# Kernel optimization log

Hardware: AMD Instinct MI355X
Metric: run time of the kernel (lower is better)

Reference implementation:

```python
import jax, jax.numpy as jnp
import numpy as np

INPUT_SIZE = 34
HIDDEN = 4
NUM_CLASSES = 3
B, T = 4096, 200


def setup_inputs() -> dict:
    key = jax.random.key(0)
    ks = jax.random.split(key, 8)
    k = 1.0 / np.sqrt(HIDDEN)  # torch default uniform init bound
    u = lambda kk, shape: jax.random.uniform(kk, shape, jnp.float32, -k, k)
    x = jax.random.normal(ks[0], (B, T, INPUT_SIZE), jnp.float32)
    W_ih = u(ks[1], (4 * HIDDEN, INPUT_SIZE))   # gate order: i, f, g, o
    W_hh = u(ks[2], (4 * HIDDEN, HIDDEN))
    b_ih = u(ks[3], (4 * HIDDEN,))
    b_hh = u(ks[4], (4 * HIDDEN,))
    W_fc = u(ks[5], (NUM_CLASSES, HIDDEN))
    b_fc = u(ks[6], (NUM_CLASSES,))
    return {"x": x, "W_ih": W_ih, "W_hh": W_hh, "b_ih": b_ih,
            "b_hh": b_hh, "W_fc": W_fc, "b_fc": b_fc}


def reference(x, W_ih, W_hh, b_ih, b_hh, W_fc, b_fc):
    Bsz = x.shape[0]
    H = W_hh.shape[1]
    # Precompute input contributions for all timesteps: [B, T, 4H]
    x_gates = jnp.einsum('btd,gd->btg', x, W_ih) + b_ih + b_hh
    x_gates = jnp.swapaxes(x_gates, 0, 1)  # [T, B, 4H] for scan

    def step(carry, xg_t):
        h, c = carry
        gates = xg_t + h @ W_hh.T          # [B, 4H]
        i, f, g, o = jnp.split(gates, 4, axis=-1)
        i = jax.nn.sigmoid(i)
        f = jax.nn.sigmoid(f)
        g = jnp.tanh(g)
        o = jax.nn.sigmoid(o)
        c = f * c + i * g
        h = o * jnp.tanh(c)
        return (h, c), None

    h0 = jnp.zeros((Bsz, H), x.dtype)
    c0 = jnp.zeros((Bsz, H), x.dtype)
    (h_last, _), _ = jax.lax.scan(step, (h0, c0), x_gates)
    # dropout is identity in eval mode
    return h_last @ W_fc.T + b_fc  # [B, num_classes]
```

## Files before the change

kernel.cpp:

```cpp
#include <hip/hip_runtime.h>
#include <hip/hip_fp16.h>

#define B_SZ 4096
#define T_SZ 200
#define IN_SZ 34
#define TILES (B_SZ * T_SZ / 64)
#define XG_BLOCKS 1024
#define WAVES_TOTAL (XG_BLOCKS * 2)
#define WT_FLOATS 560

__device__ __forceinline__ float sigf(float x) {
    return 1.0f / (1.0f + __expf(-x));
}
__device__ __forceinline__ float tanh_f(float x) {
    return 2.0f / (1.0f + __expf(-2.0f * x)) - 1.0f;
}

__device__ __forceinline__ float quad_bcast0(float v) {
    int s = __float_as_int(v);
    return __int_as_float(__builtin_amdgcn_update_dpp(s, s, 0x00, 0xf, 0xf, true));
}
__device__ __forceinline__ float quad_bcast1(float v) {
    int s = __float_as_int(v);
    return __int_as_float(__builtin_amdgcn_update_dpp(s, s, 0x55, 0xf, 0xf, true));
}
__device__ __forceinline__ float quad_bcast2(float v) {
    int s = __float_as_int(v);
    return __int_as_float(__builtin_amdgcn_update_dpp(s, s, 0xAA, 0xf, 0xf, true));
}
__device__ __forceinline__ float quad_bcast3(float v) {
    int s = __float_as_int(v);
    return __int_as_float(__builtin_amdgcn_update_dpp(s, s, 0xFF, 0xf, 0xf, true));
}

typedef const __attribute__((address_space(1))) unsigned int* gas_t;
typedef __attribute__((address_space(3))) unsigned int* las_t;

__global__ __launch_bounds__(64) void prep_kernel(
    const float* __restrict__ W_ih, const float* __restrict__ b_ih,
    const float* __restrict__ b_hh, float* __restrict__ wt) {
  for (int i = threadIdx.x; i < WT_FLOATS; i += 64) {
    if (i < 544) {
      int k = i >> 4, g = i & 15;
      wt[i] = W_ih[g * IN_SZ + k];
    } else {
      wt[i] = b_ih[i - 544] + b_hh[i - 544];
    }
  }
}

__global__ __launch_bounds__(128) void xgates_kernel(
    const float* __restrict__ x, const float* __restrict__ wt,
    __half* __restrict__ xg) {
  __shared__ float xs[2 * 2 * 64 * IN_SZ];
  const int lane = threadIdx.x & 63;
  const int wv = threadIdx.x >> 6;
  float* buf0 = &xs[wv * 2 * 64 * IN_SZ];
  float* buf1 = buf0 + 64 * IN_SZ;
  const int gw = blockIdx.x * 2 + wv;

  float bias[16];
  #pragma unroll
  for (int g = 0; g < 16; ++g) bias[g] = wt[544 + g];

  auto issue = [&](int tile, float* buf) {
    const float4* src = reinterpret_cast<const float4*>(x + (size_t)tile * 64 * IN_SZ);
    char* l = reinterpret_cast<char*>(buf);
    #pragma unroll
    for (int i = 0; i < 8; ++i)
      __builtin_amdgcn_global_load_lds((gas_t)(src + i * 64 + lane),
                                       (las_t)(l + i * 1024), 16, 0, 0);
    if (lane < 32)
      __builtin_amdgcn_global_load_lds((gas_t)(src + 512 + lane),
                                       (las_t)(l + 8192), 16, 0, 0);
  };

  int tile = gw;
  if (tile < TILES) issue(tile, buf0);
  int cur = 0;
  #pragma unroll 1
  for (; tile < TILES; tile += WAVES_TOTAL) {
    int nxt = tile + WAVES_TOTAL;
    if (nxt < TILES) {
      issue(nxt, cur ? buf0 : buf1);
      asm volatile("s_waitcnt vmcnt(9)" ::: "memory");
    } else {
      asm volatile("s_waitcnt vmcnt(0)" ::: "memory");
    }
    __builtin_amdgcn_sched_barrier(0);

    const float* buf = cur ? buf1 : buf0;
    float xr[IN_SZ];
    const float2* rp = reinterpret_cast<const float2*>(buf + lane * IN_SZ);
    #pragma unroll
    for (int k = 0; k < IN_SZ / 2; ++k) {
      float2 v = rp[k];
      xr[2 * k] = v.x;
      xr[2 * k + 1] = v.y;
    }
    float acc[16];
    #pragma unroll
    for (int g = 0; g < 16; ++g) acc[g] = bias[g];
    #pragma unroll
    for (int k = 0; k < IN_SZ; ++k) {
      #pragma unroll
      for (int g = 0; g < 16; ++g)
        acc[g] = fmaf(xr[k], wt[k * 16 + g], acc[g]);
    }
    unsigned r = (unsigned)tile * 64u + (unsigned)lane;
    unsigned bb = r / 200u;
    unsigned tt = r - bb * 200u;
    uint2* xg2 = reinterpret_cast<uint2*>(xg);
    size_t base = (size_t)bb * 800u + tt;
    #pragma unroll
    for (int j = 0; j < 4; ++j) {
      union { __half2 h[2]; uint2 v; } u;
      u.h[0] = __floats2half2_rn(acc[0 + j], acc[4 + j]);
      u.h[1] = __floats2half2_rn(acc[8 + j], acc[12 + j]);
      xg2[base + (size_t)j * 200u] = u.v;
    }
    cur ^= 1;
  }
}

#define ISSUE10(P, r)                                                          \
  asm volatile("global_load_dwordx4 %0, %[p], off\n\t"                         \
               "global_load_dwordx4 %1, %[p], off offset:16\n\t"               \
               "global_load_dwordx4 %2, %[p], off offset:32\n\t"               \
               "global_load_dwordx4 %3, %[p], off offset:48\n\t"               \
               "global_load_dwordx4 %4, %[p], off offset:64\n\t"               \
               "global_load_dwordx4 %5, %[p], off offset:80\n\t"               \
               "global_load_dwordx4 %6, %[p], off offset:96\n\t"               \
               "global_load_dwordx4 %7, %[p], off offset:112\n\t"              \
               "global_load_dwordx4 %8, %[p], off offset:128\n\t"              \
               "global_load_dwordx4 %9, %[p], off offset:144"                  \
               : "=&v"(r##0), "=&v"(r##1), "=&v"(r##2), "=&v"(r##3),           \
                 "=&v"(r##4), "=&v"(r##5), "=&v"(r##6), "=&v"(r##7),           \
                 "=&v"(r##8), "=&v"(r##9)                                      \
               : [p] "v"(P))

#define WAITV(n_)                                                              \
  do {                                                                         \
    asm volatile("s_waitcnt vmcnt(" #n_ ")" ::: "memory");                     \
    __builtin_amdgcn_sched_barrier(0);                                         \
  } while (0)

#define STEP4(v)                                                               \
  step((v).x, (v).y);                                                          \
  step((v).z, (v).w)
#define STEPS(r)                                                               \
  STEP4(r##0); STEP4(r##1); STEP4(r##2); STEP4(r##3); STEP4(r##4);             \
  STEP4(r##5); STEP4(r##6); STEP4(r##7); STEP4(r##8); STEP4(r##9)

__global__ __launch_bounds__(64) void lstm_scan(
    const __half* __restrict__ xg, const float* __restrict__ W_hh,
    const float* __restrict__ W_fc, const float* __restrict__ b_fc,
    float* __restrict__ out) {
  int tid = blockIdx.x * 64 + threadIdx.x;
  int b = tid >> 2;
  int j = tid & 3;
  float Wi[4], Wf[4], Wg[4], Wo[4];
  #pragma unroll
  for (int k = 0; k < 4; ++k) {
    Wi[k] = W_hh[(0 + j) * 4 + k];
    Wf[k] = W_hh[(4 + j) * 4 + k];
    Wg[k] = W_hh[(8 + j) * 4 + k];
    Wo[k] = W_hh[(12 + j) * 4 + k];
  }
  float h[4] = {0.f, 0.f, 0.f, 0.f};
  float c = 0.f;

  auto step = [&](unsigned lo, unsigned hi) {
    union { unsigned u; __half2 h2; } a_, b_;
    a_.u = lo;
    b_.u = hi;
    float2 p01 = __half22float2(a_.h2);
    float2 p23 = __half22float2(b_.h2);
    float pi = p01.x, pf = p01.y, pg = p23.x, po = p23.y;
    #pragma unroll
    for (int k = 0; k < 4; ++k) {
      pi = fmaf(Wi[k], h[k], pi);
      pf = fmaf(Wf[k], h[k], pf);
      pg = fmaf(Wg[k], h[k], pg);
      po = fmaf(Wo[k], h[k], po);
    }
    float iv = sigf(pi);
    float fv = sigf(pf);
    float gv = tanh_f(pg);
    float ov = sigf(po);
    c = fmaf(fv, c, iv * gv);
    float hj = ov * tanh_f(c);
    h[0] = quad_bcast0(hj);
    h[1] = quad_bcast1(hj);
    h[2] = quad_bcast2(hj);
    h[3] = quad_bcast3(hj);
  };

  const char* base = reinterpret_cast<const char*>(xg) +
                     (size_t)b * 6400 + (size_t)j * 1600;
  uint4 a0, a1, a2, a3, a4, a5, a6, a7, a8, a9;
  uint4 b0, b1, b2, b3, b4, b5, b6, b7, b8, b9;

  ISSUE10(base, a);
  ISSUE10(base + 160, b);
  const char* pa = base + 320;
  const char* pb = base + 480;

  #pragma unroll 1
  for (int it = 0; it < 4; ++it) {
    WAITV(10);
    STEPS(a);
    ISSUE10(pa, a);
    pa += 320;
    WAITV(10);
    STEPS(b);
    ISSUE10(pb, b);
    pb += 320;
  }
  WAITV(10);
  STEPS(a);
  WAITV(0);
  STEPS(b);

  if (j < 3) {
    float acc = b_fc[j];
    #pragma unroll
    for (int k = 0; k < 4; ++k) acc = fmaf(W_fc[j * 4 + k], h[k], acc);
    out[b * 3 + j] = acc;
  }
}

__global__ __launch_bounds__(256) void lstm_fused(
    const float* __restrict__ x, const float* __restrict__ W_ih,
    const float* __restrict__ W_hh, const float* __restrict__ b_ih,
    const float* __restrict__ b_hh, const float* __restrict__ W_fc,
    const float* __restrict__ b_fc, float* __restrict__ out) {
  __shared__ float Ws[16 * IN_SZ];
  for (int i = threadIdx.x; i < 16 * IN_SZ; i += 256) Ws[i] = W_ih[i];
  __syncthreads();
  int tid = blockIdx.x * 256 + threadIdx.x;
  int b = tid >> 2;
  int j = tid & 3;
  float bi = b_ih[0 + j] + b_hh[0 + j];
  float bf = b_ih[4 + j] + b_hh[4 + j];
  float bg = b_ih[8 + j] + b_hh[8 + j];
  float bo = b_ih[12 + j] + b_hh[12 + j];
  float Wi[4], Wf[4], Wg[4], Wo[4];
  #pragma unroll
  for (int k = 0; k < 4; ++k) {
    Wi[k] = W_hh[(0 + j) * 4 + k];
    Wf[k] = W_hh[(4 + j) * 4 + k];
    Wg[k] = W_hh[(8 + j) * 4 + k];
    Wo[k] = W_hh[(12 + j) * 4 + k];
  }
  float h[4] = {0.f, 0.f, 0.f, 0.f};
  float c = 0.f;
  const float2* xp = reinterpret_cast<const float2*>(x + (size_t)b * T_SZ * IN_SZ);
  int lbase = (threadIdx.x & 63) & ~3;
  for (int t = 0; t < T_SZ; ++t) {
    float xr[IN_SZ];
    #pragma unroll
    for (int k = 0; k < IN_SZ / 2; ++k) {
      float2 v = xp[(size_t)t * (IN_SZ / 2) + k];
      xr[2 * k] = v.x;
      xr[2 * k + 1] = v.y;
    }
    float pi = bi, pf = bf, pg = bg, po = bo;
    #pragma unroll
    for (int k = 0; k < IN_SZ; ++k) {
      pi = fmaf(xr[k], Ws[(0 + j) * IN_SZ + k], pi);
      pf = fmaf(xr[k], Ws[(4 + j) * IN_SZ + k], pf);
      pg = fmaf(xr[k], Ws[(8 + j) * IN_SZ + k], pg);
      po = fmaf(xr[k], Ws[(12 + j) * IN_SZ + k], po);
    }
    #pragma unroll
    for (int k = 0; k < 4; ++k) {
      pi = fmaf(Wi[k], h[k], pi);
      pf = fmaf(Wf[k], h[k], pf);
      pg = fmaf(Wg[k], h[k], pg);
      po = fmaf(Wo[k], h[k], po);
    }
    float iv = sigf(pi);
    float fv = sigf(pf);
    float gv = tanh_f(pg);
    float ov = sigf(po);
    c = fmaf(fv, c, iv * gv);
    float hj = ov * tanh_f(c);
    h[0] = __shfl(hj, lbase + 0);
    h[1] = __shfl(hj, lbase + 1);
    h[2] = __shfl(hj, lbase + 2);
    h[3] = __shfl(hj, lbase + 3);
  }
  if (j < 3) {
    float acc = b_fc[j];
    #pragma unroll
    for (int k = 0; k < 4; ++k) acc = fmaf(W_fc[j * 4 + k], h[k], acc);
    out[b * 3 + j] = acc;
  }
}

extern "C" void kernel_launch(void* const* d_in, const int* in_sizes, int n_in,
                              void* d_out, int out_size, void* d_ws, size_t ws_size,
                              hipStream_t stream) {
  const float* x    = (const float*)d_in[0];
  const float* W_ih = (const float*)d_in[1];
  const float* W_hh = (const float*)d_in[2];
  const float* b_ih = (const float*)d_in[3];
  const float* b_hh = (const float*)d_in[4];
  const float* W_fc = (const float*)d_in[5];
  const float* b_fc = (const float*)d_in[6];
  float* out = (float*)d_out;

  const size_t xg_off = 4096;
  const size_t need = xg_off + (size_t)B_SZ * T_SZ * 16 * sizeof(__half);
  if (ws_size >= need) {
    float* wt = (float*)d_ws;
    __half* xg = (__half*)((char*)d_ws + xg_off);
    hipLaunchKernelGGL(prep_kernel, dim3(1), dim3(64), 0, stream,
                       W_ih, b_ih, b_hh, wt);
    hipLaunchKernelGGL(xgates_kernel, dim3(XG_BLOCKS), dim3(128), 0, stream,
                       x, wt, xg);
    hipLaunchKernelGGL(lstm_scan, dim3(B_SZ * 4 / 64), dim3(64), 0, stream,
                       xg, W_hh, W_fc, b_fc, out);
  } else {
    hipLaunchKernelGGL(lstm_fused, dim3(B_SZ * 4 / 256), dim3(256), 0, stream,
                       x, W_ih, W_hh, b_ih, b_hh, W_fc, b_fc, out);
  }
}
```

Before: 82.29 us.

## Replace LDS-staged x-gates loads with direct per-thread register double-buffered loads

The x-gates projection kernel no longer stages 64-row tiles through LDS via global_load_lds. Instead, each thread handles four rows spaced a grid apart and loads each 136-byte row straight into registers with 17 dwordx2 loads, double-buffered across two register sets with explicit vmcnt waits. The goal is to remove the LDS round trip and the persistent-loop overhead. The trade-off is uncoalesced, strided per-lane global loads and very high register pressure. The scan kernel also gains a launch_bounds minimum-blocks hint.

```diff
diff --git a/kernel.cpp b/kernel.cpp
--- a/kernel.cpp
+++ b/kernel.cpp
@@ -4,10 +4,10 @@
 #define B_SZ 4096
 #define T_SZ 200
 #define IN_SZ 34
-#define TILES (B_SZ * T_SZ / 64)
-#define XG_BLOCKS 1024
-#define WAVES_TOTAL (XG_BLOCKS * 2)
 #define WT_FLOATS 560
+#define XG_THREADS 204800
+
+typedef __attribute__((ext_vector_type(2))) float f32x2;
 
 __device__ __forceinline__ float sigf(float x) {
     return 1.0f / (1.0f + __expf(-x));
@@ -32,9 +32,6 @@
     int s = __float_as_int(v);
     return __int_as_float(__builtin_amdgcn_update_dpp(s, s, 0xFF, 0xf, 0xf, true));
 }
-
-typedef const __attribute__((address_space(1))) unsigned int* gas_t;
-typedef __attribute__((address_space(3))) unsigned int* las_t;
 
 __global__ __launch_bounds__(64) void prep_kernel(
     const float* __restrict__ W_ih, const float* __restrict__ b_ih,
@@ -49,68 +46,79 @@
   }
 }
 
-__global__ __launch_bounds__(128) void xgates_kernel(
+#define WAITV(n_)                                                              \
+  do {                                                                         \
+    asm volatile("s_waitcnt vmcnt(" #n_ ")" ::: "memory");                     \
+    __builtin_amdgcn_sched_barrier(0);                                         \
+  } while (0)
+
+#define ISSUE17(P, r)                                                          \
+  asm volatile("global_load_dwordx2 %0, %[p], off\n\t"                         \
+               "global_load_dwordx2 %1, %[p], off offset:8\n\t"                \
+               "global_load_dwordx2 %2, %[p], off offset:16\n\t"               \
+               "global_load_dwordx2 %3, %[p], off offset:24\n\t"               \
+               "global_load_dwordx2 %4, %[p], off offset:32\n\t"               \
+               "global_load_dwordx2 %5, %[p], off offset:40\n\t"               \
+               "global_load_dwordx2 %6, %[p], off offset:48\n\t"               \
+               "global_load_dwordx2 %7, %[p], off offset:56\n\t"               \
+               "global_load_dwordx2 %8, %[p], off offset:64\n\t"               \
+               "global_load_dwordx2 %9, %[p], off offset:72\n\t"               \
+               "global_load_dwordx2 %10, %[p], off offset:80\n\t"              \
+               "global_load_dwordx2 %11, %[p], off offset:88\n\t"              \
+               "global_load_dwordx2 %12, %[p], off offset:96\n\t"              \
+               "global_load_dwordx2 %13, %[p], off offset:104\n\t"             \
+               "global_load_dwordx2 %14, %[p], off offset:112\n\t"             \
+               "global_load_dwordx2 %15, %[p], off offset:120\n\t"             \
+               "global_load_dwordx2 %16, %[p], off offset:128"                 \
+               : "=&v"(r##0), "=&v"(r##1), "=&v"(r##2), "=&v"(r##3),           \
+                 "=&v"(r##4), "=&v"(r##5), "=&v"(r##6), "=&v"(r##7),           \
+                 "=&v"(r##8), "=&v"(r##9), "=&v"(r##10), "=&v"(r##11),         \
+                 "=&v"(r##12), "=&v"(r##13), "=&v"(r##14), "=&v"(r##15),       \
+                 "=&v"(r##16)                                                  \
+               : [p] "v"(P))
+
+#define FMA2(vv, kk)                                                           \
+  do {                                                                         \
+    _Pragma("unroll") for (int g = 0; g < 16; ++g)                             \
+        acc[g] = fmaf((vv).x, wt[(2 * (kk)) * 16 + g], acc[g]);                \
+    _Pragma("unroll") for (int g = 0; g < 16; ++g)                             \
+        acc[g] = fmaf((vv).y, wt[(2 * (kk) + 1) * 16 + g], acc[g]);            \
+  } while (0)
+
+#define ROWCOMP(r)                                                             \
+  do {                                                                         \
+    FMA2(r##0, 0); FMA2(r##1, 1); FMA2(r##2, 2); FMA2(r##3, 3);                \
+    FMA2(r##4, 4); FMA2(r##5, 5); FMA2(r##6, 6); FMA2(r##7, 7);                \
+    FMA2(r##8, 8); FMA2(r##9, 9); FMA2(r##10, 10); FMA2(r##11, 11);            \
+    FMA2(r##12, 12); FMA2(r##13, 13); FMA2(r##14, 14); FMA2(r##15, 15);        \
+    _Pragma("unroll") for (int g = 0; g < 16; ++g)                             \
+        acc[g] = fmaf((r##16).x, wt[32 * 16 + g], acc[g]);                     \
+    _Pragma("unroll") for (int g = 0; g < 16; ++g)                             \
+        acc[g] = fmaf((r##16).y, wt[33 * 16 + g], acc[g]);                     \
+  } while (0)
+
+__global__ __launch_bounds__(256, 1) void xgates_kernel(
     const float* __restrict__ x, const float* __restrict__ wt,
     __half* __restrict__ xg) {
-  __shared__ float xs[2 * 2 * 64 * IN_SZ];
-  const int lane = threadIdx.x & 63;
-  const int wv = threadIdx.x >> 6;
-  float* buf0 = &xs[wv * 2 * 64 * IN_SZ];
-  float* buf1 = buf0 + 64 * IN_SZ;
-  const int gw = blockIdx.x * 2 + wv;
+  const unsigned g0 = blockIdx.x * 256 + threadIdx.x;
 
   float bias[16];
   #pragma unroll
-  for (int g = 0; g < 16; ++g) bias[g] = wt[544 + g];
-
-  auto issue = [&](int tile, float* buf) {
-    const float4* src = reinterpret_cast<const float4*>(x + (size_t)tile * 64 * IN_SZ);
-    char* l = reinterpret_cast<char*>(buf);
-    #pragma unroll
-    for (int i = 0; i < 8; ++i)
-      __builtin_amdgcn_global_load_lds((gas_t)(src + i * 64 + lane),
-                                       (las_t)(l + i * 1024), 16, 0, 0);
-    if (lane < 32)
-      __builtin_amdgcn_global_load_lds((gas_t)(src + 512 + lane),
-                                       (las_t)(l + 8192), 16, 0, 0);
+  for (int gg = 0; gg < 16; ++gg) bias[gg] = wt[544 + gg];
+
+  f32x2 A0, A1, A2, A3, A4, A5, A6, A7, A8, A9, A10, A11, A12, A13, A14, A15, A16;
+  f32x2 B0, B1, B2, B3, B4, B5, B6, B7, B8, B9, B10, B11, B12, B13, B14, B15, B16;
+
+  const char* xb = reinterpret_cast<const char*>(x);
+  uint2* xg2 = reinterpret_cast<uint2*>(xg);
+
+  auto rowaddr = [&](int q) {
+    return xb + (size_t)(g0 + (unsigned)q * XG_THREADS) * 136;
   };
-
-  int tile = gw;
-  if (tile < TILES) issue(tile, buf0);
-  int cur = 0;
-  #pragma unroll 1
-  for (; tile < TILES; tile += WAVES_TOTAL) {
-    int nxt = tile + WAVES_TOTAL;
-    if (nxt < TILES) {
-      issue(nxt, cur ? buf0 : buf1);
-      asm volatile("s_waitcnt vmcnt(9)" ::: "memory");
-    } else {
-      asm volatile("s_waitcnt vmcnt(0)" ::: "memory");
-    }
-    __builtin_amdgcn_sched_barrier(0);
-
-    const float* buf = cur ? buf1 : buf0;
-    float xr[IN_SZ];
-    const float2* rp = reinterpret_cast<const float2*>(buf + lane * IN_SZ);
-    #pragma unroll
-    for (int k = 0; k < IN_SZ / 2; ++k) {
-      float2 v = rp[k];
-      xr[2 * k] = v.x;
-      xr[2 * k + 1] = v.y;
-    }
-    float acc[16];
-    #pragma unroll
-    for (int g = 0; g < 16; ++g) acc[g] = bias[g];
-    #pragma unroll
-    for (int k = 0; k < IN_SZ; ++k) {
-      #pragma unroll
-      for (int g = 0; g < 16; ++g)
-        acc[g] = fmaf(xr[k], wt[k * 16 + g], acc[g]);
-    }
-    unsigned r = (unsigned)tile * 64u + (unsigned)lane;
+  auto store_gates = [&](int q, const float* acc) {
+    unsigned r = g0 + (unsigned)q * XG_THREADS;
     unsigned bb = r / 200u;
     unsigned tt = r - bb * 200u;
-    uint2* xg2 = reinterpret_cast<uint2*>(xg);
     size_t base = (size_t)bb * 800u + tt;
     #pragma unroll
     for (int j = 0; j < 4; ++j) {
@@ -119,8 +127,34 @@
       u.h[1] = __floats2half2_rn(acc[8 + j], acc[12 + j]);
       xg2[base + (size_t)j * 200u] = u.v;
     }
-    cur ^= 1;
-  }
+  };
+
+  float acc[16];
+
+  ISSUE17(rowaddr(0), A);
+  ISSUE17(rowaddr(1), B);
+  WAITV(17);
+  #pragma unroll
+  for (int gg = 0; gg < 16; ++gg) acc[gg] = bias[gg];
+  ROWCOMP(A);
+  store_gates(0, acc);
+  ISSUE17(rowaddr(2), A);
+  WAITV(21);
+  #pragma unroll
+  for (int gg = 0; gg < 16; ++gg) acc[gg] = bias[gg];
+  ROWCOMP(B);
+  store_gates(1, acc);
+  ISSUE17(rowaddr(3), B);
+  WAITV(21);
+  #pragma unroll
+  for (int gg = 0; gg < 16; ++gg) acc[gg] = bias[gg];
+  ROWCOMP(A);
+  store_gates(2, acc);
+  WAITV(4);
+  #pragma unroll
+  for (int gg = 0; gg < 16; ++gg) acc[gg] = bias[gg];
+  ROWCOMP(B);
+  store_gates(3, acc);
 }
 
 #define ISSUE10(P, r)                                                          \
@@ -139,12 +173,6 @@
                  "=&v"(r##8), "=&v"(r##9)                                      \
                : [p] "v"(P))
 
-#define WAITV(n_)                                                              \
-  do {                                                                         \
-    asm volatile("s_waitcnt vmcnt(" #n_ ")" ::: "memory");                     \
-    __builtin_amdgcn_sched_barrier(0);                                         \
-  } while (0)
-
 #define STEP4(v)                                                               \
   step((v).x, (v).y);                                                          \
   step((v).z, (v).w)
@@ -152,7 +180,7 @@
   STEP4(r##0); STEP4(r##1); STEP4(r##2); STEP4(r##3); STEP4(r##4);             \
   STEP4(r##5); STEP4(r##6); STEP4(r##7); STEP4(r##8); STEP4(r##9)
 
-__global__ __launch_bounds__(64) void lstm_scan(
+__global__ __launch_bounds__(64, 1) void lstm_scan(
     const __half* __restrict__ xg, const float* __restrict__ W_hh,
     const float* __restrict__ W_fc, const float* __restrict__ b_fc,
     float* __restrict__ out) {
@@ -318,7 +346,7 @@
     __half* xg = (__half*)((char*)d_ws + xg_off);
     hipLaunchKernelGGL(prep_kernel, dim3(1), dim3(64), 0, stream,
                        W_ih, b_ih, b_hh, wt);
-    hipLaunchKernelGGL(xgates_kernel, dim3(XG_BLOCKS), dim3(128), 0, stream,
+    hipLaunchKernelGGL(xgates_kernel, dim3(XG_THREADS / 256), dim3(256), 0, stream,
                        x, wt, xg);
     hipLaunchKernelGGL(lstm_scan, dim3(B_SZ * 4 / 64), dim3(64), 0, stream,
                        xg, W_hh, W_fc, b_fc, out);
```

Result: slower. 100.9 us (+22.6%).

## Interleave xgates layout per batch group and stage scan loads through LDS

Applied to the files above, without the earlier changes.

The xgates kernel now writes its fp16 gate values in a layout grouped by 16 batch rows, with every 2 timesteps forming a contiguous 1KB chunk across the group's 64 lanes. The scan kernel uses global_load_lds to bring these chunks into double-buffered shared memory, so each wave issues fully coalesced loads in place of per-lane strided 16-byte loads. This is meant to improve memory access efficiency in the latency-bound recurrent scan. The cost is an extra LDS read per step, and the wait counts must still match how many global_load_lds operations are outstanding.

```diff
diff --git a/kernel.cpp b/kernel.cpp
--- a/kernel.cpp
+++ b/kernel.cpp
@@ -35,6 +35,12 @@
 
 typedef const __attribute__((address_space(1))) unsigned int* gas_t;
 typedef __attribute__((address_space(3))) unsigned int* las_t;
+
+#define WAITV(n_)                                                              \
+  do {                                                                         \
+    asm volatile("s_waitcnt vmcnt(" #n_ ")" ::: "memory");                     \
+    __builtin_amdgcn_sched_barrier(0);                                         \
+  } while (0)
 
 __global__ __launch_bounds__(64) void prep_kernel(
     const float* __restrict__ W_ih, const float* __restrict__ b_ih,
@@ -110,55 +116,33 @@
     unsigned r = (unsigned)tile * 64u + (unsigned)lane;
     unsigned bb = r / 200u;
     unsigned tt = r - bb * 200u;
-    uint2* xg2 = reinterpret_cast<uint2*>(xg);
-    size_t base = (size_t)bb * 800u + tt;
+    unsigned bg = bb >> 4;
+    unsigned ln0 = (bb & 15u) * 4u;
+    unsigned p = tt >> 1;
+    unsigned half = tt & 1u;
+    char* ob = reinterpret_cast<char*>(xg) +
+               (size_t)bg * 102400 + (size_t)p * 1024 + half * 8;
     #pragma unroll
     for (int j = 0; j < 4; ++j) {
       union { __half2 h[2]; uint2 v; } u;
       u.h[0] = __floats2half2_rn(acc[0 + j], acc[4 + j]);
       u.h[1] = __floats2half2_rn(acc[8 + j], acc[12 + j]);
-      xg2[base + (size_t)j * 200u] = u.v;
+      *reinterpret_cast<uint2*>(ob + (size_t)(ln0 + j) * 16) = u.v;
     }
     cur ^= 1;
   }
 }
-
-#define ISSUE10(P, r)                                                          \
-  asm volatile("global_load_dwordx4 %0, %[p], off\n\t"                         \
-               "global_load_dwordx4 %1, %[p], off offset:16\n\t"               \
-               "global_load_dwordx4 %2, %[p], off offset:32\n\t"               \
-               "global_load_dwordx4 %3, %[p], off offset:48\n\t"               \
-               "global_load_dwordx4 %4, %[p], off offset:64\n\t"               \
-               "global_load_dwordx4 %5, %[p], off offset:80\n\t"               \
-               "global_load_dwordx4 %6, %[p], off offset:96\n\t"               \
-               "global_load_dwordx4 %7, %[p], off offset:112\n\t"              \
-               "global_load_dwordx4 %8, %[p], off offset:128\n\t"              \
-               "global_load_dwordx4 %9, %[p], off offset:144"                  \
-               : "=&v"(r##0), "=&v"(r##1), "=&v"(r##2), "=&v"(r##3),           \
-                 "=&v"(r##4), "=&v"(r##5), "=&v"(r##6), "=&v"(r##7),           \
-                 "=&v"(r##8), "=&v"(r##9)                                      \
-               : [p] "v"(P))
-
-#define WAITV(n_)                                                              \
-  do {                                                                         \
-    asm volatile("s_waitcnt vmcnt(" #n_ ")" ::: "memory");                     \
-    __builtin_amdgcn_sched_barrier(0);                                         \
-  } while (0)
-
-#define STEP4(v)                                                               \
-  step((v).x, (v).y);                                                          \
-  step((v).z, (v).w)
-#define STEPS(r)                                                               \
-  STEP4(r##0); STEP4(r##1); STEP4(r##2); STEP4(r##3); STEP4(r##4);             \
-  STEP4(r##5); STEP4(r##6); STEP4(r##7); STEP4(r##8); STEP4(r##9)
 
 __global__ __launch_bounds__(64) void lstm_scan(
     const __half* __restrict__ xg, const float* __restrict__ W_hh,
     const float* __restrict__ W_fc, const float* __restrict__ b_fc,
     float* __restrict__ out) {
-  int tid = blockIdx.x * 64 + threadIdx.x;
-  int b = tid >> 2;
-  int j = tid & 3;
+  __shared__ __align__(16) char lds[2][10240];
+  const int lane = threadIdx.x;
+  const int bg = blockIdx.x;
+  const int j = lane & 3;
+  const int b = bg * 16 + (lane >> 2);
+
   float Wi[4], Wf[4], Wg[4], Wo[4];
   #pragma unroll
   for (int k = 0; k < 4; ++k) {
@@ -196,31 +180,37 @@
     h[3] = quad_bcast3(hj);
   };
 
-  const char* base = reinterpret_cast<const char*>(xg) +
-                     (size_t)b * 6400 + (size_t)j * 1600;
-  uint4 a0, a1, a2, a3, a4, a5, a6, a7, a8, a9;
-  uint4 b0, b1, b2, b3, b4, b5, b6, b7, b8, b9;
-
-  ISSUE10(base, a);
-  ISSUE10(base + 160, b);
-  const char* pa = base + 320;
-  const char* pb = base + 480;
-
+  const char* gbase = reinterpret_cast<const char*>(xg) + (size_t)bg * 102400;
+  auto issue = [&](int n, int bufid) {
+    const char* p = gbase + (size_t)n * 10240 + (size_t)lane * 16;
+    char* l = lds[bufid];
+    #pragma unroll
+    for (int u = 0; u < 10; ++u)
+      __builtin_amdgcn_global_load_lds((gas_t)(p + u * 1024),
+                                       (las_t)(l + u * 1024), 16, 0, 0);
+  };
+  auto compute = [&](int bufid) {
+    const char* l = lds[bufid] + (size_t)lane * 16;
+    #pragma unroll
+    for (int u = 0; u < 10; ++u) {
+      uint4 v = *reinterpret_cast<const uint4*>(l + u * 1024);
+      step(v.x, v.y);
+      step(v.z, v.w);
+    }
+  };
+
+  issue(0, 0);
+  issue(1, 1);
   #pragma unroll 1
-  for (int it = 0; it < 4; ++it) {
+  for (int n = 0; n < 8; ++n) {
     WAITV(10);
-    STEPS(a);
-    ISSUE10(pa, a);
-    pa += 320;
-    WAITV(10);
-    STEPS(b);
-    ISSUE10(pb, b);
-    pb += 320;
+    compute(n & 1);
+    issue(n + 2, n & 1);
   }
   WAITV(10);
-  STEPS(a);
+  compute(0);
   WAITV(0);
-  STEPS(b);
+  compute(1);
 
   if (j < 3) {
     float acc = b_fc[j];
@@ -320,7 +310,7 @@
                        W_ih, b_ih, b_hh, wt);
     hipLaunchKernelGGL(xgates_kernel, dim3(XG_BLOCKS), dim3(128), 0, stream,
                        x, wt, xg);
-    hipLaunchKernelGGL(lstm_scan, dim3(B_SZ * 4 / 64), dim3(64), 0, stream,
+    hipLaunchKernelGGL(lstm_scan, dim3(B_SZ / 16), dim3(64), 0, stream,
                        xg, W_hh, W_fc, b_fc, out);
   } else {
     hipLaunchKernelGGL(lstm_fused, dim3(B_SZ * 4 / 256), dim3(256), 0, stream,
```

After: 141.2 us. +71.5%, slower.
